# Kernel tuning notes

Hardware: AMD Instinct MI355X
Metric: run time of the kernel (lower is better)

## Reference

```python
import jax, jax.numpy as jnp
import numpy as np

TAU = 0.1
MASK_VAL = 1e9


def setup_inputs() -> dict:
    key = jax.random.key(0)
    ka, kb = jax.random.split(key)
    B, D = 4096, 512
    return {
        "view_a": jax.random.normal(ka, (B, D), dtype=jnp.float32),
        "view_b": jax.random.normal(kb, (B, D), dtype=jnp.float32),
    }


def _l2norm(x):
    return x / jnp.maximum(jnp.linalg.norm(x, axis=-1, keepdims=True), 1e-12)


def reference(view_a, view_b):
    a = _l2norm(view_a)
    b = _l2norm(view_b)
    B = a.shape[0]
    labels = jnp.arange(B)  # start_i = 0 (single device)
    mask = jnp.eye(B, dtype=a.dtype) * MASK_VAL

    logits_aa = a @ a.T / TAU - mask
    logits_bb = b @ b.T / TAU - mask
    logits_ab = a @ b.T / TAU
    logits_ba = b @ a.T / TAU

    full_a = jnp.concatenate([logits_ab, logits_aa], axis=1)  # [B, 2B]
    full_b = jnp.concatenate([logits_ba, logits_bb], axis=1)

    def ce(logits):
        logp = jax.nn.log_softmax(logits, axis=-1)
        return -jnp.mean(jnp.take_along_axis(logp, labels[:, None], axis=-1))

    loss = (ce(full_a) + ce(full_b)) / 2

    pred = jnp.argmax(full_a, axis=-1)
    acc = 100.0 * jnp.sum(pred == labels) / B
    return loss, acc
```

## Files before the change

kernel.cpp:

```cpp
#include <hip/hip_runtime.h>
#include <stdint.h>


#define BN 4096
#define DK 512
#define NSPLIT 16
#define NEG_BIG -1e30f
#define SCL 0.15625f
#define SCL2 0.225396744f
#define C2 14.4269504f
#define TILE_BYTES (32 * DK)

typedef __attribute__((ext_vector_type(16))) float floatx16;
typedef __attribute__((ext_vector_type(8))) int intx8;

__global__ void __launch_bounds__(256) prep_kernel(
    const float* __restrict__ A, const float* __restrict__ Bv,
    unsigned char* __restrict__ An, unsigned char* __restrict__ Bn,
    float* __restrict__ diag, float* __restrict__ out) {
  if (blockIdx.x == 0 && threadIdx.x < 2) out[threadIdx.x] = 0.0f;
  const int w = threadIdx.x >> 6, lane = threadIdx.x & 63;
  const int row = blockIdx.x * 4 + w;
  const float4* pa4 = (const float4*)(A + (size_t)row * DK);
  const float4* pb4 = (const float4*)(Bv + (size_t)row * DK);
  float4 a0 = pa4[lane * 2], a1 = pa4[lane * 2 + 1];
  float4 b0 = pb4[lane * 2], b1 = pb4[lane * 2 + 1];
  float ssa = a0.x * a0.x + a0.y * a0.y + a0.z * a0.z + a0.w * a0.w +
              a1.x * a1.x + a1.y * a1.y + a1.z * a1.z + a1.w * a1.w;
  float ssb = b0.x * b0.x + b0.y * b0.y + b0.z * b0.z + b0.w * b0.w +
              b1.x * b1.x + b1.y * b1.y + b1.z * b1.z + b1.w * b1.w;
  float sab = a0.x * b0.x + a0.y * b0.y + a0.z * b0.z + a0.w * b0.w +
              a1.x * b1.x + a1.y * b1.y + a1.z * b1.z + a1.w * b1.w;
#pragma unroll
  for (int off = 32; off > 0; off >>= 1) {
    ssa += __shfl_xor(ssa, off);
    ssb += __shfl_xor(ssb, off);
    sab += __shfl_xor(sab, off);
  }
  float na = fmaxf(sqrtf(ssa), 1e-12f);
  float nb = fmaxf(sqrtf(ssb), 1e-12f);
  const float s = 8.0f;
  float sa = s / na, sb = s / nb;
  const int doff = (lane >> 2) * 32 + (lane & 1) * 16 + ((lane >> 1) & 1) * 8;
  {
    int v0 = __builtin_amdgcn_cvt_pk_fp8_f32(a0.x * sa, a0.y * sa, 0, false);
    v0 = __builtin_amdgcn_cvt_pk_fp8_f32(a0.z * sa, a0.w * sa, v0, true);
    int v1 = __builtin_amdgcn_cvt_pk_fp8_f32(a1.x * sa, a1.y * sa, 0, false);
    v1 = __builtin_amdgcn_cvt_pk_fp8_f32(a1.z * sa, a1.w * sa, v1, true);
    int2 pv; pv.x = v0; pv.y = v1;
    *(int2*)(An + (size_t)row * DK + doff) = pv;
  }
  {
    int v0 = __builtin_amdgcn_cvt_pk_fp8_f32(b0.x * sb, b0.y * sb, 0, false);
    v0 = __builtin_amdgcn_cvt_pk_fp8_f32(b0.z * sb, b0.w * sb, v0, true);
    int v1 = __builtin_amdgcn_cvt_pk_fp8_f32(b1.x * sb, b1.y * sb, 0, false);
    v1 = __builtin_amdgcn_cvt_pk_fp8_f32(b1.z * sb, b1.w * sb, v1, true);
    int2 pv; pv.x = v0; pv.y = v1;
    *(int2*)(Bn + (size_t)row * DK + doff) = pv;
  }
  if (lane == 0) diag[row] = (sab / (na * nb)) * 10.0f;
}

__global__ void __launch_bounds__(256, 2) tiles_kernel(
    const unsigned char* __restrict__ An, const unsigned char* __restrict__ Bn,
    float* __restrict__ pSA, float* __restrict__ pMA, float* __restrict__ pSB) {
  __shared__ __align__(16) unsigned char smem[2 * TILE_BYTES];

  const int rb = blockIdx.x;
  const int split = blockIdx.y;
  const int tid = threadIdx.x;
  const int lane = tid & 63, w = tid >> 6;
  const int n5 = lane & 31, h = lane >> 5;
  const int r0 = rb * 128;
  const int myrow = r0 + w * 32 + n5;

  intx8 awA[8], awB[8];
  {
    const unsigned char* pA = An + (size_t)myrow * DK + h * 16;
    const unsigned char* pB = Bn + (size_t)myrow * DK + h * 16;
#pragma unroll
    for (int i = 0; i < 8; ++i) {
      int4 c0 = *(const int4*)(pA + i * 64);
      int4 c1 = *(const int4*)(pA + i * 64 + 32);
      intx8 v = {c0.x, c0.y, c0.z, c0.w, c1.x, c1.y, c1.z, c1.w};
      awA[i] = v;
      c0 = *(const int4*)(pB + i * 64);
      c1 = *(const int4*)(pB + i * 64 + 32);
      intx8 u = {c0.x, c0.y, c0.z, c0.w, c1.x, c1.y, c1.z, c1.w};
      awB[i] = u;
    }
  }

  float lA[16], lB[16], mx[16];
#pragma unroll
  for (int r = 0; r < 16; ++r) { lA[r] = 0.f; lB[r] = 0.f; mx[r] = NEG_BIG; }

  auto stage = [&](unsigned char* buf, int jt) {
    const unsigned char* csrc = (jt < 128) ? An : Bn;
    const int cb = (jt & 127) * 32;
#pragma unroll
    for (int ii = 0; ii < 4; ++ii) {
      const int cp = w * 4 + ii;
      const int cl = cp * 2 + h;
      const unsigned char* src =
          csrc + (size_t)(cb + cl) * DK + ((n5 ^ (cl & 7)) * 16);
      __builtin_amdgcn_global_load_lds(
          (const __attribute__((address_space(1))) void*)src,
          (__attribute__((address_space(3))) void*)(buf + cp * 1024),
          16, 0, 0);
    }
  };

  stage(smem, split * 16);
  __syncthreads();

  const int swz = n5 & 7;
  for (int u = 0; u < 16; ++u) {
    const int jt = split * 16 + u;
    unsigned char* cur = smem + (u & 1) * TILE_BYTES;
    unsigned char* nxt = smem + ((u + 1) & 1) * TILE_BYTES;
    if (u < 15) stage(nxt, jt + 1);

    floatx16 accA, accB;
#pragma unroll
    for (int r = 0; r < 16; ++r) { accA[r] = 0.f; accB[r] = 0.f; }

    const unsigned char* bbase = cur + (size_t)n5 * DK;
#pragma unroll
    for (int i = 0; i < 8; ++i) {
      const int p1 = ((4 * i + h) ^ swz) * 16;
      const int p2 = ((4 * i + 2 + h) ^ swz) * 16;
      int4 b0 = *(const int4*)(bbase + p1);
      int4 b1 = *(const int4*)(bbase + p2);
      intx8 bw = {b0.x, b0.y, b0.z, b0.w, b1.x, b1.y, b1.z, b1.w};
      accA = __builtin_amdgcn_mfma_scale_f32_32x32x64_f8f6f4(
          awA[i], bw, accA, 0, 0, 0, 0x7F7F7F7F, 0, 0x7F7F7F7F);
      accB = __builtin_amdgcn_mfma_scale_f32_32x32x64_f8f6f4(
          awB[i], bw, accB, 0, 0, 0, 0x7F7F7F7F, 0, 0x7F7F7F7F);
    }

    const bool dtile = (((jt & 127) >> 2) == rb);
    const int colbase = (jt & 127) * 32;
#pragma unroll
    for (int r = 0; r < 16; ++r) {
      float vA = accA[r], vB = accB[r];
      if (dtile) {
        const int rowg = r0 + w * 32 + (r & 3) + 8 * (r >> 2) + 4 * h;
        if (rowg == colbase + n5) { vA = NEG_BIG; vB = NEG_BIG; }
      }
      mx[r] = fmaxf(mx[r], vA);
      lA[r] += exp2f(fmaf(vA, SCL2, -C2));
      lB[r] += exp2f(fmaf(vB, SCL2, -C2));
    }
    __syncthreads();
  }

#pragma unroll
  for (int off = 1; off < 32; off <<= 1)
#pragma unroll
    for (int r = 0; r < 16; ++r) {
      lA[r] += __shfl_xor(lA[r], off);
      lB[r] += __shfl_xor(lB[r], off);
      mx[r] = fmaxf(mx[r], __shfl_xor(mx[r], off));
    }
  if (n5 == 0) {
#pragma unroll
    for (int r = 0; r < 16; ++r) {
      const int row = r0 + w * 32 + (r & 3) + 8 * (r >> 2) + 4 * h;
      pSA[split * BN + row] = lA[r];
      pMA[split * BN + row] = mx[r] * SCL;
      pSB[split * BN + row] = lB[r];
    }
  }
}

__global__ void __launch_bounds__(256) finalize_kernel(
    const float* __restrict__ pSA, const float* __restrict__ pMA,
    const float* __restrict__ pSB, const float* __restrict__ diag,
    float* __restrict__ out) {
  const int row = blockIdx.x * 256 + threadIdx.x;
  float SA = 0.f, SB = 0.f, MA = NEG_BIG;
#pragma unroll
  for (int s = 0; s < NSPLIT; ++s) {
    SA += pSA[s * BN + row];
    SB += pSB[s * BN + row];
    MA = fmaxf(MA, pMA[s * BN + row]);
  }
  const float d = diag[row];
  const float eL = exp2f(fmaf(d, 1.44269504f, -C2));
  float lseA = 10.0f + logf(SA + eL);
  float lseB = 10.0f + logf(SB + eL);
  float lossi = (lseA - d) + (lseB - d);
  float corr = (d >= MA) ? 1.f : 0.f;
#pragma unroll
  for (int off = 32; off > 0; off >>= 1) {
    lossi += __shfl_xor(lossi, off);
    corr += __shfl_xor(corr, off);
  }
  __shared__ float sred[2][4];
  if ((threadIdx.x & 63) == 0) {
    int w = threadIdx.x >> 6;
    sred[0][w] = lossi; sred[1][w] = corr;
  }
  __syncthreads();
  if (threadIdx.x == 0) {
    float ls = sred[0][0] + sred[0][1] + sred[0][2] + sred[0][3];
    float cs = sred[1][0] + sred[1][1] + sred[1][2] + sred[1][3];
    atomicAdd(&out[0], ls * (1.0f / 8192.0f));
    atomicAdd(&out[1], cs * (100.0f / 4096.0f));
  }
}

extern "C" void kernel_launch(void* const* d_in, const int* in_sizes, int n_in,
                              void* d_out, int out_size, void* d_ws, size_t ws_size,
                              hipStream_t stream) {
  const float* A = (const float*)d_in[0];
  const float* Bv = (const float*)d_in[1];
  unsigned char* An = (unsigned char*)d_ws;
  unsigned char* Bn = An + (size_t)BN * DK;
  float* diag = (float*)(Bn + (size_t)BN * DK);
  float* pSA = diag + BN;
  float* pMA = pSA + NSPLIT * BN;
  float* pSB = pMA + NSPLIT * BN;
  float* out = (float*)d_out;

  prep_kernel<<<BN / 4, 256, 0, stream>>>(A, Bv, An, Bn, diag, out);
  tiles_kernel<<<dim3(32, 16), 256, 0, stream>>>(An, Bn, pSA, pMA, pSB);
  finalize_kernel<<<BN / 256, 256, 0, stream>>>(pSA, pMA, pSB, diag, out);
}
```

Baseline: 124.1 us.

## Exploit Gram-matrix symmetry: compute upper-triangular blocks, accumulate row stats via atomics

The tile kernel now covers only the upper-triangular 128x128 block pairs. Each off-diagonal block contributes both row sums and, through the transposed view, column sums, so the matmul and exp work roughly halves. Per-split partial buffers are replaced by global atomicAdd sums and an atomicMax row maximum on a biased float-as-uint encoding. Finalize then reads single accumulators. In exchange it adds atomic contention, a serial block-index decode loop, and an extra small launch to zero the output.

Result: slower. 164.3 us (+32.4%).

```diff
diff --git a/kernel.cpp b/kernel.cpp
--- a/kernel.cpp
+++ b/kernel.cpp
@@ -4,7 +4,7 @@
 
 #define BN 4096
 #define DK 512
-#define NSPLIT 16
+#define NB 32
 #define NEG_BIG -1e30f
 #define SCL 0.15625f
 #define SCL2 0.225396744f
@@ -17,8 +17,11 @@
 __global__ void __launch_bounds__(256) prep_kernel(
     const float* __restrict__ A, const float* __restrict__ Bv,
     unsigned char* __restrict__ An, unsigned char* __restrict__ Bn,
-    float* __restrict__ diag, float* __restrict__ out) {
-  if (blockIdx.x == 0 && threadIdx.x < 2) out[threadIdx.x] = 0.0f;
+    float* __restrict__ diag, float* __restrict__ zero_region) {
+  {
+    const int idx = blockIdx.x * 256 + threadIdx.x;
+    if (idx < 3 * BN) zero_region[idx] = 0.0f;
+  }
   const int w = threadIdx.x >> 6, lane = threadIdx.x & 63;
   const int row = blockIdx.x * 4 + w;
   const float4* pa4 = (const float4*)(A + (size_t)row * DK);
@@ -63,16 +66,23 @@
 
 __global__ void __launch_bounds__(256, 2) tiles_kernel(
     const unsigned char* __restrict__ An, const unsigned char* __restrict__ Bn,
-    float* __restrict__ pSA, float* __restrict__ pMA, float* __restrict__ pSB) {
+    float* __restrict__ accLA, float* __restrict__ accLB,
+    unsigned* __restrict__ accMA) {
   __shared__ __align__(16) unsigned char smem[2 * TILE_BYTES];
 
-  const int rb = blockIdx.x;
-  const int split = blockIdx.y;
+  int p = blockIdx.x >> 1;
+  const int v = blockIdx.x & 1;
+  int bi = 0;
+  while (p >= NB - bi) { p -= NB - bi; ++bi; }
+  const int bj = bi + p;
+  const bool diagb = (bi == bj);
+
   const int tid = threadIdx.x;
   const int lane = tid & 63, w = tid >> 6;
   const int n5 = lane & 31, h = lane >> 5;
-  const int r0 = rb * 128;
+  const int r0 = bi * 128;
   const int myrow = r0 + w * 32 + n5;
+  const int c0 = bj * 128;
 
   intx8 awA[8], awB[8];
   {
@@ -80,14 +90,14 @@
     const unsigned char* pB = Bn + (size_t)myrow * DK + h * 16;
 #pragma unroll
     for (int i = 0; i < 8; ++i) {
-      int4 c0 = *(const int4*)(pA + i * 64);
-      int4 c1 = *(const int4*)(pA + i * 64 + 32);
-      intx8 v = {c0.x, c0.y, c0.z, c0.w, c1.x, c1.y, c1.z, c1.w};
-      awA[i] = v;
-      c0 = *(const int4*)(pB + i * 64);
-      c1 = *(const int4*)(pB + i * 64 + 32);
-      intx8 u = {c0.x, c0.y, c0.z, c0.w, c1.x, c1.y, c1.z, c1.w};
-      awB[i] = u;
+      int4 q0 = *(const int4*)(pA + i * 64);
+      int4 q1 = *(const int4*)(pA + i * 64 + 32);
+      intx8 va = {q0.x, q0.y, q0.z, q0.w, q1.x, q1.y, q1.z, q1.w};
+      awA[i] = va;
+      q0 = *(const int4*)(pB + i * 64);
+      q1 = *(const int4*)(pB + i * 64 + 32);
+      intx8 vb = {q0.x, q0.y, q0.z, q0.w, q1.x, q1.y, q1.z, q1.w};
+      awB[i] = vb;
     }
   }
 
@@ -95,9 +105,9 @@
 #pragma unroll
   for (int r = 0; r < 16; ++r) { lA[r] = 0.f; lB[r] = 0.f; mx[r] = NEG_BIG; }
 
-  auto stage = [&](unsigned char* buf, int jt) {
-    const unsigned char* csrc = (jt < 128) ? An : Bn;
-    const int cb = (jt & 127) * 32;
+  const unsigned char* csrc = (v == 0) ? An : Bn;
+  auto stage = [&](unsigned char* buf, int t) {
+    const int cb = c0 + t * 32;
 #pragma unroll
     for (int ii = 0; ii < 4; ++ii) {
       const int cp = w * 4 + ii;
@@ -111,15 +121,14 @@
     }
   };
 
-  stage(smem, split * 16);
+  stage(smem, 0);
   __syncthreads();
 
   const int swz = n5 & 7;
-  for (int u = 0; u < 16; ++u) {
-    const int jt = split * 16 + u;
-    unsigned char* cur = smem + (u & 1) * TILE_BYTES;
-    unsigned char* nxt = smem + ((u + 1) & 1) * TILE_BYTES;
-    if (u < 15) stage(nxt, jt + 1);
+  for (int t = 0; t < 4; ++t) {
+    unsigned char* cur = smem + (t & 1) * TILE_BYTES;
+    unsigned char* nxt = smem + ((t + 1) & 1) * TILE_BYTES;
+    if (t < 3) stage(nxt, t + 1);
 
     floatx16 accA, accB;
 #pragma unroll
@@ -130,27 +139,42 @@
     for (int i = 0; i < 8; ++i) {
       const int p1 = ((4 * i + h) ^ swz) * 16;
       const int p2 = ((4 * i + 2 + h) ^ swz) * 16;
-      int4 b0 = *(const int4*)(bbase + p1);
-      int4 b1 = *(const int4*)(bbase + p2);
-      intx8 bw = {b0.x, b0.y, b0.z, b0.w, b1.x, b1.y, b1.z, b1.w};
+      int4 q0 = *(const int4*)(bbase + p1);
+      int4 q1 = *(const int4*)(bbase + p2);
+      intx8 bw = {q0.x, q0.y, q0.z, q0.w, q1.x, q1.y, q1.z, q1.w};
       accA = __builtin_amdgcn_mfma_scale_f32_32x32x64_f8f6f4(
           awA[i], bw, accA, 0, 0, 0, 0x7F7F7F7F, 0, 0x7F7F7F7F);
       accB = __builtin_amdgcn_mfma_scale_f32_32x32x64_f8f6f4(
           awB[i], bw, accB, 0, 0, 0, 0x7F7F7F7F, 0, 0x7F7F7F7F);
     }
 
-    const bool dtile = (((jt & 127) >> 2) == rb);
-    const int colbase = (jt & 127) * 32;
+    const int colbase = c0 + t * 32;
+    float cS = 0.f, cM = NEG_BIG;
 #pragma unroll
     for (int r = 0; r < 16; ++r) {
       float vA = accA[r], vB = accB[r];
-      if (dtile) {
+      if (diagb) {
         const int rowg = r0 + w * 32 + (r & 3) + 8 * (r >> 2) + 4 * h;
         if (rowg == colbase + n5) { vA = NEG_BIG; vB = NEG_BIG; }
       }
       mx[r] = fmaxf(mx[r], vA);
-      lA[r] += exp2f(fmaf(vA, SCL2, -C2));
-      lB[r] += exp2f(fmaf(vB, SCL2, -C2));
+      float eA = exp2f(fmaf(vA, SCL2, -C2));
+      float eB = exp2f(fmaf(vB, SCL2, -C2));
+      lA[r] += eA;
+      lB[r] += eB;
+      cS += eA + eB;
+      if (v == 0) cM = fmaxf(cM, fmaxf(vA, vB));
+    }
+    if (!diagb) {
+      cS += __shfl_xor(cS, 32);
+      if (v == 0) cM = fmaxf(cM, __shfl_xor(cM, 32));
+      if (h == 0) {
+        float* dst = v ? accLB : accLA;
+        atomicAdd(&dst[colbase + n5], cS);
+        if (v == 0)
+          atomicMax(&accMA[colbase + n5],
+                    __float_as_uint(cM * SCL + 20.0f));
+      }
     }
     __syncthreads();
   }
@@ -167,30 +191,23 @@
 #pragma unroll
     for (int r = 0; r < 16; ++r) {
       const int row = r0 + w * 32 + (r & 3) + 8 * (r >> 2) + 4 * h;
-      pSA[split * BN + row] = lA[r];
-      pMA[split * BN + row] = mx[r] * SCL;
-      pSB[split * BN + row] = lB[r];
+      atomicAdd(&accLA[row], lA[r]);
+      atomicAdd(&accLB[row], lB[r]);
+      atomicMax(&accMA[row], __float_as_uint(mx[r] * SCL + 20.0f));
     }
   }
 }
 
 __global__ void __launch_bounds__(256) finalize_kernel(
-    const float* __restrict__ pSA, const float* __restrict__ pMA,
-    const float* __restrict__ pSB, const float* __restrict__ diag,
+    const float* __restrict__ accLA, const float* __restrict__ accLB,
+    const unsigned* __restrict__ accMA, const float* __restrict__ diag,
     float* __restrict__ out) {
   const int row = blockIdx.x * 256 + threadIdx.x;
-  float SA = 0.f, SB = 0.f, MA = NEG_BIG;
-#pragma unroll
-  for (int s = 0; s < NSPLIT; ++s) {
-    SA += pSA[s * BN + row];
-    SB += pSB[s * BN + row];
-    MA = fmaxf(MA, pMA[s * BN + row]);
-  }
+  const float SA = accLA[row], SB = accLB[row];
+  const float MA = __uint_as_float(accMA[row]) - 20.0f;
   const float d = diag[row];
   const float eL = exp2f(fmaf(d, 1.44269504f, -C2));
-  float lseA = 10.0f + logf(SA + eL);
-  float lseB = 10.0f + logf(SB + eL);
-  float lossi = (lseA - d) + (lseB - d);
+  float lossi = (10.0f + logf(SA + eL) - d) + (10.0f + logf(SB + eL) - d);
   float corr = (d >= MA) ? 1.f : 0.f;
 #pragma unroll
   for (int off = 32; off > 0; off >>= 1) {
@@ -209,6 +226,10 @@
     atomicAdd(&out[0], ls * (1.0f / 8192.0f));
     atomicAdd(&out[1], cs * (100.0f / 4096.0f));
   }
+}
+
+__global__ void zero_out_kernel(float* out) {
+  if (threadIdx.x < 2) out[threadIdx.x] = 0.0f;
 }
 
 extern "C" void kernel_launch(void* const* d_in, const int* in_sizes, int n_in,
@@ -219,12 +240,13 @@
   unsigned char* An = (unsigned char*)d_ws;
   unsigned char* Bn = An + (size_t)BN * DK;
   float* diag = (float*)(Bn + (size_t)BN * DK);
-  float* pSA = diag + BN;
-  float* pMA = pSA + NSPLIT * BN;
-  float* pSB = pMA + NSPLIT * BN;
+  float* accLA = diag + BN;
+  float* accLB = accLA + BN;
+  unsigned* accMA = (unsigned*)(accLB + BN);
   float* out = (float*)d_out;
 
-  prep_kernel<<<BN / 4, 256, 0, stream>>>(A, Bv, An, Bn, diag, out);
-  tiles_kernel<<<dim3(32, 16), 256, 0, stream>>>(An, Bn, pSA, pMA, pSB);
-  finalize_kernel<<<BN / 256, 256, 0, stream>>>(pSA, pMA, pSB, diag, out);
-}
+  zero_out_kernel<<<1, 64, 0, stream>>>(out);
+  prep_kernel<<<BN / 4, 256, 0, stream>>>(A, Bv, An, Bn, diag, accLA);
+  tiles_kernel<<<NB * (NB + 1), 256, 0, stream>>>(An, Bn, accLA, accLB, accMA);
+  finalize_kernel<<<BN / 256, 256, 0, stream>>>(accLA, accLB, accMA, diag, out);
+}
```
